# Optimization experiments

Hardware: AMD Instinct MI355X
Metric: run time of the kernel (lower is better)

Reference implementation:

```python
import jax, jax.numpy as jnp
import numpy as np

FRAME_LEN = 512
FRAME_HOP = 256
EPSILON = float(np.finfo(np.float32).eps)


def _dft_kernels(frame_len=FRAME_LEN):
    # Matches torch: K = view_as_real(fft.rfft(eye(N), dim=1))[:frame_len], windowed by hann.
    # rfft of delta at t gives exp(-2pi i f t / N): real = cos, imag = -sin.
    N = frame_len  # already a power of two
    n = jnp.arange(frame_len, dtype=jnp.float32)
    window = 0.5 * (1.0 - jnp.cos(2.0 * jnp.pi * n / frame_len))  # periodic hann
    f = jnp.arange(N // 2 + 1, dtype=jnp.float32)  # 257 bins
    ang = 2.0 * jnp.pi * f[:, None] * n[None, :] / N  # [F, L]
    Kr = jnp.cos(ang) * window
    Ki = -jnp.sin(ang) * window  # torch rfft imaginary part
    return Kr, Ki


def _frame(x, frame_len=FRAME_LEN, hop=FRAME_HOP):
    B, Ns = x.shape
    T = (Ns - frame_len) // hop + 1
    idx = jnp.arange(T)[:, None] * hop + jnp.arange(frame_len)[None, :]  # [T, L]
    return x[:, idx]  # [B, T, L]


def reference(x):
    Kr, Ki = _dft_kernels()
    xf = _frame(x)  # [B, T, L]
    r = jnp.einsum('btl,fl->bft', xf, Kr)       # real part of conv1d output
    i = -jnp.einsum('btl,fl->bft', xf, Ki)      # i = -imag (as in torch code)
    mag = jnp.sqrt(r * r + i * i)               # B x F x T
    f = jnp.clip(mag, EPSILON, None)
    mean = jnp.mean(f, axis=-1, keepdims=True)
    std = jnp.std(f, axis=-1, keepdims=True, ddof=1)  # torch std is unbiased
    feat = (f - mean) / (std + EPSILON)
    return mag, feat


def setup_inputs() -> dict:
    key = jax.random.key(0)
    x = jax.random.normal(key, (64, 160000), dtype=jnp.float32)
    return {"x": x}
```

## Files before the change

kernel.cpp:

```cpp
#include <hip/hip_runtime.h>
#include <math.h>

#define FRAME_LEN 512
#define HOP       256
#define NFREQ     257
#define NBATCH    64
#define NSAMP     160000
#define NSAMPH    80000
#define TFRAMES   624
#define EPS       1.1920928955078125e-07f

#define MT 128
#define FT 32
#define BK 64
#define KH 256
#define XBLKS 5000

#define ASZ (MT * BK)
#define BSZ (2 * FT * BK)

typedef __attribute__((ext_vector_type(8))) short short8;
typedef __attribute__((ext_vector_type(4))) float f32x4;

static __device__ __forceinline__ unsigned int f2bf(float f) {
    unsigned int u = __float_as_uint(f);
    return (u + 0x7fffu + ((u >> 16) & 1u)) >> 16;
}
static __device__ __forceinline__ void gload_lds16(const void* g, void* l) {
    __builtin_amdgcn_global_load_lds(
        (const __attribute__((address_space(1))) void*)g,
        (__attribute__((address_space(3))) void*)l, 16, 0, 0);
}

__global__ __launch_bounds__(256) void prep(const float* __restrict__ x,
                                            unsigned short* __restrict__ xe,
                                            unsigned short* __restrict__ xo,
                                            unsigned short* __restrict__ Wec,
                                            unsigned short* __restrict__ Wes,
                                            unsigned short* __restrict__ Woc,
                                            unsigned short* __restrict__ Wos) {
    if (blockIdx.x < XBLKS) {
        int i = blockIdx.x * 256 + threadIdx.x;
        const float4* src = (const float4*)x + (size_t)i * 2;
        float4 a = src[0], b = src[1];
        uint2 e, o;
        e.x = f2bf(a.x) | (f2bf(a.z) << 16);
        e.y = f2bf(b.x) | (f2bf(b.z) << 16);
        o.x = f2bf(a.y) | (f2bf(a.w) << 16);
        o.y = f2bf(b.y) | (f2bf(b.w) << 16);
        *(uint2*)(xe + (size_t)i * 4) = e;
        *(uint2*)(xo + (size_t)i * 4) = o;
    } else {
        int f = blockIdx.x - XBLKS;
        int n2 = threadIdx.x;
        unsigned short ec = 0, es = 0, oc = 0, os = 0;
        if (f <= 128) {
            int ne = 2 * n2, no = 2 * n2 + 1;
            float we = 0.5f * (1.0f - cosf(2.0f * (float)M_PI * (float)ne / (float)FRAME_LEN));
            float wo = 0.5f * (1.0f - cosf(2.0f * (float)M_PI * (float)no / (float)FRAME_LEN));
            float ange = (float)((f * ne) & (FRAME_LEN - 1)) * (2.0f * (float)M_PI / (float)FRAME_LEN);
            float ango = (float)((f * no) & (FRAME_LEN - 1)) * (2.0f * (float)M_PI / (float)FRAME_LEN);
            float se_, ce_, so_, co_;
            sincosf(ange, &se_, &ce_);
            sincosf(ango, &so_, &co_);
            ec = (unsigned short)f2bf(ce_ * we);
            es = (unsigned short)f2bf(se_ * we);
            oc = (unsigned short)f2bf(co_ * wo);
            os = (unsigned short)f2bf(so_ * wo);
        }
        Wec[f * KH + n2] = ec; Wes[f * KH + n2] = es;
        Woc[f * KH + n2] = oc; Wos[f * KH + n2] = os;
    }
}

__global__ __launch_bounds__(256) void stft_mfma(
    const unsigned short* __restrict__ xe, const unsigned short* __restrict__ xo,
    const unsigned short* __restrict__ Wec, const unsigned short* __restrict__ Wes,
    const unsigned short* __restrict__ Woc, const unsigned short* __restrict__ Wos,
    float* __restrict__ mag)
{
    __shared__ unsigned short As[2][MT][BK];
    __shared__ unsigned short Bs[2][2][FT][BK];

    const int tid = threadIdx.x;
    const int logical = ((int)blockIdx.x & 7) * 195 + ((int)blockIdx.x >> 3);
    const int tileM = logical / 5;
    const int tileF = logical % 5;
    const int wid = tid >> 6;
    const int lane = tid & 63;
    const int lrow = lane & 15;
    const int lhi = lane >> 4;

    unsigned short* AsB = &As[0][0][0];
    unsigned short* BsB = &Bs[0][0][0][0];

    const unsigned short* pA[2][4];
    #pragma unroll
    for (int j = 0; j < 4; j++) {
        int idx = wid * 4 + j;
        int row = idx * 8 + (lane >> 3);
        int m = tileM * MT + row;
        int b = m / TFRAMES;
        int t = m - b * TFRAMES;
        int chunk = (lane & 7) ^ (row & 7);
        size_t off = (size_t)b * NSAMPH + t * (HOP / 2) + chunk * 8;
        pA[0][j] = xe + off;
        pA[1][j] = xo + off;
    }
    const unsigned short* pB[2][2];
    #pragma unroll
    for (int j = 0; j < 2; j++) {
        int i = wid * 2 + j;
        int row = (i & 3) * 8 + (lane >> 3);
        int fg = tileF * FT + row;
        int chunk = (lane & 7) ^ (row & 7);
        size_t off = (size_t)fg * KH + chunk * 8;
        pB[0][j] = ((i & 4) ? Wes : Wec) + off;
        pB[1][j] = ((i & 4) ? Wos : Woc) + off;
    }

    f32x4 aC[2][2][2] = {};
    f32x4 aS[2][2][2] = {};

    #pragma unroll
    for (int j = 0; j < 4; j++)
        gload_lds16(pA[0][j], AsB + (wid * 4 + j) * 512);
    #pragma unroll
    for (int j = 0; j < 2; j++)
        gload_lds16(pB[0][j], BsB + (wid * 2 + j) * 512);
    __syncthreads();

    int buf = 0;
    #pragma unroll
    for (int it = 0; it < 8; it++) {
        const int p = it >> 2;
        if (it < 7) {
            const int pn = (it + 1) >> 2;
            const int k0 = ((it + 1) & 3) * BK;
            #pragma unroll
            for (int j = 0; j < 4; j++)
                gload_lds16(pA[pn][j] + k0, AsB + (buf ^ 1) * ASZ + (wid * 4 + j) * 512);
            #pragma unroll
            for (int j = 0; j < 2; j++)
                gload_lds16(pB[pn][j] + k0, BsB + (buf ^ 1) * BSZ + (wid * 2 + j) * 512);
        }
        #pragma unroll
        for (int ks = 0; ks < 2; ks++) {
            short8 a[2], bc[2], bsn[2];
            const int c = (ks * 4 + lhi) ^ (lrow & 7);
            #pragma unroll
            for (int mf = 0; mf < 2; mf++)
                a[mf] = *(const short8*)(AsB + buf * ASZ +
                    (wid * 32 + mf * 16 + lrow) * BK + c * 8);
            #pragma unroll
            for (int nf = 0; nf < 2; nf++) {
                bc[nf]  = *(const short8*)(BsB + buf * BSZ +
                    (nf * 16 + lrow) * BK + c * 8);
                bsn[nf] = *(const short8*)(BsB + buf * BSZ + FT * BK +
                    (nf * 16 + lrow) * BK + c * 8);
            }
            #pragma unroll
            for (int mf = 0; mf < 2; mf++) {
                #pragma unroll
                for (int nf = 0; nf < 2; nf++) {
                    aC[p][mf][nf] = __builtin_amdgcn_mfma_f32_16x16x32_bf16(
                        a[mf], bc[nf], aC[p][mf][nf], 0, 0, 0);
                    aS[p][mf][nf] = __builtin_amdgcn_mfma_f32_16x16x32_bf16(
                        a[mf], bsn[nf], aS[p][mf][nf], 0, 0, 0);
                }
            }
        }
        __syncthreads();
        buf ^= 1;
    }

    #pragma unroll
    for (int mf = 0; mf < 2; mf++) {
        int m0 = tileM * MT + wid * 32 + mf * 16 + lhi * 4;
        int b = m0 / TFRAMES;
        int t = m0 - b * TFRAMES;
        #pragma unroll
        for (int nf = 0; nf < 2; nf++) {
            int f = tileF * FT + nf * 16 + lrow;
            float4 od, om;
            #pragma unroll
            for (int q = 0; q < 4; q++) {
                const float Ce = aC[0][mf][nf][q], Co = aC[1][mf][nf][q];
                const float Se = aS[0][mf][nf][q], So = aS[1][mf][nf][q];
                const float rd = Ce + Co, id = Se + So;
                const float rm = Ce - Co, im = So - Se;
                (&od.x)[q] = sqrtf(rd * rd + id * id);
                (&om.x)[q] = sqrtf(rm * rm + im * im);
            }
            if (f <= 128)
                *(float4*)(mag + ((size_t)b * NFREQ + f) * TFRAMES + t) = od;
            if (f <= 127)
                *(float4*)(mag + ((size_t)b * NFREQ + (256 - f)) * TFRAMES + t) = om;
        }
    }
}

__global__ __launch_bounds__(256) void normalize(const float* __restrict__ mag,
                                                 float* __restrict__ feat)
{
    const int row = blockIdx.x * 4 + (threadIdx.x >> 6);
    const int lane = threadIdx.x & 63;
    const float* mp = mag + (size_t)row * TFRAMES;

    float4 v[3];
    float sum = 0.f;
    #pragma unroll
    for (int i = 0; i < 3; i++) {
        int c4 = lane + i * 64;
        if (c4 < TFRAMES / 4) {
            float4 t = *(const float4*)(mp + c4 * 4);
            t.x = fmaxf(t.x, EPS); t.y = fmaxf(t.y, EPS);
            t.z = fmaxf(t.z, EPS); t.w = fmaxf(t.w, EPS);
            v[i] = t;
            sum += (t.x + t.y) + (t.z + t.w);
        } else {
            v[i] = make_float4(0.f, 0.f, 0.f, 0.f);
        }
    }
    #pragma unroll
    for (int off = 1; off < 64; off <<= 1) sum += __shfl_xor(sum, off, 64);
    const float mean = sum * (1.0f / (float)TFRAMES);

    float ssd = 0.f;
    #pragma unroll
    for (int i = 0; i < 3; i++) {
        int c4 = lane + i * 64;
        if (c4 < TFRAMES / 4) {
            float dx = v[i].x - mean, dy = v[i].y - mean;
            float dz = v[i].z - mean, dw = v[i].w - mean;
            ssd += (dx * dx + dy * dy) + (dz * dz + dw * dw);
        }
    }
    #pragma unroll
    for (int off = 1; off < 64; off <<= 1) ssd += __shfl_xor(ssd, off, 64);
    const float stdv = sqrtf(ssd * (1.0f / (float)(TFRAMES - 1)));
    const float inv = 1.0f / (stdv + EPS);

    float* fp = feat + (size_t)row * TFRAMES;
    #pragma unroll
    for (int i = 0; i < 3; i++) {
        int c4 = lane + i * 64;
        if (c4 < TFRAMES / 4) {
            float4 o;
            o.x = (v[i].x - mean) * inv; o.y = (v[i].y - mean) * inv;
            o.z = (v[i].z - mean) * inv; o.w = (v[i].w - mean) * inv;
            *(float4*)(fp + c4 * 4) = o;
        }
    }
}

extern "C" void kernel_launch(void* const* d_in, const int* in_sizes, int n_in,
                              void* d_out, int out_size, void* d_ws, size_t ws_size,
                              hipStream_t stream) {
    const float* x = (const float*)d_in[0];
    unsigned short* Wec = (unsigned short*)d_ws;
    unsigned short* Wes = Wec + 160 * KH;
    unsigned short* Woc = Wes + 160 * KH;
    unsigned short* Wos = Woc + 160 * KH;
    unsigned short* xe  = Wos + 160 * KH;
    unsigned short* xo  = xe + (size_t)NBATCH * NSAMPH;
    float* mag  = (float*)d_out;
    float* feat = mag + (size_t)NBATCH * NFREQ * TFRAMES;

    prep<<<XBLKS + 160, 256, 0, stream>>>(x, xe, xo, Wec, Wes, Woc, Wos);

    stft_mfma<<<312 * 5, 256, 0, stream>>>(xe, xo, Wec, Wes, Woc, Wos, mag);

    normalize<<<NBATCH * NFREQ / 4, 256, 0, stream>>>(mag, feat);
}
```

Before: 54.40 us.

## Stage A tiles through registers with two-deep prefetch and widen prep conversion

The STFT GEMM kernel stops using direct global-to-LDS loads for the signal tile. It now loads the A tile into registers two iterations ahead, writes it into swizzled LDS after compute, and uses manual waitcnt and barriers so the loads overlap the MFMA work. The B tile still uses direct LDS loads, one stage ahead. The kernel also gains an occupancy hint (launch_bounds 256,3), and the bf16 prep kernel now handles 16 floats per thread with half as many blocks. This adds register pressure and relies on hand-written vmcnt counting that must match the load order exactly.

```diff
diff --git a/kernel.cpp b/kernel.cpp
--- a/kernel.cpp
+++ b/kernel.cpp
@@ -14,7 +14,7 @@
 #define FT 32
 #define BK 64
 #define KH 256
-#define XBLKS 5000
+#define XBLKS 2500
 
 #define ASZ (MT * BK)
 #define BSZ (2 * FT * BK)
@@ -41,15 +41,19 @@
                                             unsigned short* __restrict__ Wos) {
     if (blockIdx.x < XBLKS) {
         int i = blockIdx.x * 256 + threadIdx.x;
-        const float4* src = (const float4*)x + (size_t)i * 2;
-        float4 a = src[0], b = src[1];
-        uint2 e, o;
-        e.x = f2bf(a.x) | (f2bf(a.z) << 16);
-        e.y = f2bf(b.x) | (f2bf(b.z) << 16);
-        o.x = f2bf(a.y) | (f2bf(a.w) << 16);
-        o.y = f2bf(b.y) | (f2bf(b.w) << 16);
-        *(uint2*)(xe + (size_t)i * 4) = e;
-        *(uint2*)(xo + (size_t)i * 4) = o;
+        const float4* src = (const float4*)x + (size_t)i * 4;
+        float4 v0 = src[0], v1 = src[1], v2 = src[2], v3 = src[3];
+        uint4 e, o;
+        e.x = f2bf(v0.x) | (f2bf(v0.z) << 16);
+        e.y = f2bf(v1.x) | (f2bf(v1.z) << 16);
+        e.z = f2bf(v2.x) | (f2bf(v2.z) << 16);
+        e.w = f2bf(v3.x) | (f2bf(v3.z) << 16);
+        o.x = f2bf(v0.y) | (f2bf(v0.w) << 16);
+        o.y = f2bf(v1.y) | (f2bf(v1.w) << 16);
+        o.z = f2bf(v2.y) | (f2bf(v2.w) << 16);
+        o.w = f2bf(v3.y) | (f2bf(v3.w) << 16);
+        *(uint4*)(xe + (size_t)i * 8) = e;
+        *(uint4*)(xo + (size_t)i * 8) = o;
     } else {
         int f = blockIdx.x - XBLKS;
         int n2 = threadIdx.x;
@@ -73,7 +77,7 @@
     }
 }
 
-__global__ __launch_bounds__(256) void stft_mfma(
+__global__ __launch_bounds__(256, 3) void stft_mfma(
     const unsigned short* __restrict__ xe, const unsigned short* __restrict__ xo,
     const unsigned short* __restrict__ Wec, const unsigned short* __restrict__ Wes,
     const unsigned short* __restrict__ Woc, const unsigned short* __restrict__ Wos,
@@ -95,17 +99,17 @@
     unsigned short* BsB = &Bs[0][0][0][0];
 
     const unsigned short* pA[2][4];
+    int wAo[4];
     #pragma unroll
     for (int j = 0; j < 4; j++) {
-        int idx = wid * 4 + j;
-        int row = idx * 8 + (lane >> 3);
-        int m = tileM * MT + row;
+        int r = (wid * 4 + j) * 8 + (lane >> 3);
+        int m = tileM * MT + r;
         int b = m / TFRAMES;
         int t = m - b * TFRAMES;
-        int chunk = (lane & 7) ^ (row & 7);
-        size_t off = (size_t)b * NSAMPH + t * (HOP / 2) + chunk * 8;
+        size_t off = (size_t)b * NSAMPH + t * (HOP / 2) + (lane & 7) * 8;
         pA[0][j] = xe + off;
         pA[1][j] = xo + off;
+        wAo[j] = r * (BK * 2) + ((((lane & 7) ^ (r & 7))) << 4);
     }
     const unsigned short* pB[2][2];
     #pragma unroll
@@ -121,57 +125,88 @@
 
     f32x4 aC[2][2][2] = {};
     f32x4 aS[2][2][2] = {};
-
+    uint4 R0[4], R1[4];
+
+    #pragma unroll
+    for (int j = 0; j < 4; j++) R0[j] = *(const uint4*)(pA[0][j]);
+    __builtin_amdgcn_sched_barrier(0);
+    #pragma unroll
+    for (int j = 0; j < 2; j++) gload_lds16(pB[0][j], BsB + (wid * 2 + j) * 512);
+    __builtin_amdgcn_sched_barrier(0);
+    #pragma unroll
+    for (int j = 0; j < 4; j++) R1[j] = *(const uint4*)(pA[0][j] + BK);
     #pragma unroll
     for (int j = 0; j < 4; j++)
-        gload_lds16(pA[0][j], AsB + (wid * 4 + j) * 512);
-    #pragma unroll
-    for (int j = 0; j < 2; j++)
-        gload_lds16(pB[0][j], BsB + (wid * 2 + j) * 512);
-    __syncthreads();
-
-    int buf = 0;
-    #pragma unroll
-    for (int it = 0; it < 8; it++) {
-        const int p = it >> 2;
-        if (it < 7) {
-            const int pn = (it + 1) >> 2;
-            const int k0 = ((it + 1) & 3) * BK;
-            #pragma unroll
-            for (int j = 0; j < 4; j++)
-                gload_lds16(pA[pn][j] + k0, AsB + (buf ^ 1) * ASZ + (wid * 4 + j) * 512);
+        *(uint4*)((char*)AsB + wAo[j]) = R0[j];
+    asm volatile("s_waitcnt vmcnt(4) lgkmcnt(0)" ::: "memory");
+    __builtin_amdgcn_s_barrier();
+    __builtin_amdgcn_sched_barrier(0);
+
+    #pragma unroll
+    for (int c = 0; c < 8; c++) {
+        if (c + 1 < 8) {
+            const int pn = (c + 1) >> 2, kn = ((c + 1) & 3) * BK;
             #pragma unroll
             for (int j = 0; j < 2; j++)
-                gload_lds16(pB[pn][j] + k0, BsB + (buf ^ 1) * BSZ + (wid * 2 + j) * 512);
-        }
-        #pragma unroll
-        for (int ks = 0; ks < 2; ks++) {
-            short8 a[2], bc[2], bsn[2];
-            const int c = (ks * 4 + lhi) ^ (lrow & 7);
+                gload_lds16(pB[pn][j] + kn,
+                            BsB + ((c + 1) & 1) * BSZ + (wid * 2 + j) * 512);
+        }
+        __builtin_amdgcn_sched_barrier(0);
+        if (c + 2 < 8) {
+            const int p2 = (c + 2) >> 2, k2 = ((c + 2) & 3) * BK;
+            if ((c & 1) == 0) {
+                #pragma unroll
+                for (int j = 0; j < 4; j++) R0[j] = *(const uint4*)(pA[p2][j] + k2);
+            } else {
+                #pragma unroll
+                for (int j = 0; j < 4; j++) R1[j] = *(const uint4*)(pA[p2][j] + k2);
+            }
+        }
+        {
+            const int p = c >> 2, bo = c & 1;
             #pragma unroll
-            for (int mf = 0; mf < 2; mf++)
-                a[mf] = *(const short8*)(AsB + buf * ASZ +
-                    (wid * 32 + mf * 16 + lrow) * BK + c * 8);
-            #pragma unroll
-            for (int nf = 0; nf < 2; nf++) {
-                bc[nf]  = *(const short8*)(BsB + buf * BSZ +
-                    (nf * 16 + lrow) * BK + c * 8);
-                bsn[nf] = *(const short8*)(BsB + buf * BSZ + FT * BK +
-                    (nf * 16 + lrow) * BK + c * 8);
-            }
-            #pragma unroll
-            for (int mf = 0; mf < 2; mf++) {
+            for (int ks = 0; ks < 2; ks++) {
+                short8 a[2], bc[2], bsn[2];
+                const int ci = (ks * 4 + lhi) ^ (lrow & 7);
+                #pragma unroll
+                for (int mf = 0; mf < 2; mf++)
+                    a[mf] = *(const short8*)(AsB + bo * ASZ +
+                        (wid * 32 + mf * 16 + lrow) * BK + ci * 8);
                 #pragma unroll
                 for (int nf = 0; nf < 2; nf++) {
-                    aC[p][mf][nf] = __builtin_amdgcn_mfma_f32_16x16x32_bf16(
-                        a[mf], bc[nf], aC[p][mf][nf], 0, 0, 0);
-                    aS[p][mf][nf] = __builtin_amdgcn_mfma_f32_16x16x32_bf16(
-                        a[mf], bsn[nf], aS[p][mf][nf], 0, 0, 0);
+                    bc[nf]  = *(const short8*)(BsB + bo * BSZ +
+                        (nf * 16 + lrow) * BK + ci * 8);
+                    bsn[nf] = *(const short8*)(BsB + bo * BSZ + FT * BK +
+                        (nf * 16 + lrow) * BK + ci * 8);
+                }
+                #pragma unroll
+                for (int mf = 0; mf < 2; mf++) {
+                    #pragma unroll
+                    for (int nf = 0; nf < 2; nf++) {
+                        aC[p][mf][nf] = __builtin_amdgcn_mfma_f32_16x16x32_bf16(
+                            a[mf], bc[nf], aC[p][mf][nf], 0, 0, 0);
+                        aS[p][mf][nf] = __builtin_amdgcn_mfma_f32_16x16x32_bf16(
+                            a[mf], bsn[nf], aS[p][mf][nf], 0, 0, 0);
+                    }
                 }
             }
         }
-        __syncthreads();
-        buf ^= 1;
+        if (c < 7) {
+            const int wb = (c + 1) & 1;
+            if ((c & 1) == 0) {
+                #pragma unroll
+                for (int j = 0; j < 4; j++)
+                    *(uint4*)((char*)AsB + wb * (ASZ * 2) + wAo[j]) = R1[j];
+            } else {
+                #pragma unroll
+                for (int j = 0; j < 4; j++)
+                    *(uint4*)((char*)AsB + wb * (ASZ * 2) + wAo[j]) = R0[j];
+            }
+            if (c < 6) asm volatile("s_waitcnt vmcnt(4) lgkmcnt(0)" ::: "memory");
+            else       asm volatile("s_waitcnt vmcnt(0) lgkmcnt(0)" ::: "memory");
+            __builtin_amdgcn_s_barrier();
+            __builtin_amdgcn_sched_barrier(0);
+        }
     }
 
     #pragma unroll
```

New measurement: 56.76 us. +4.3%, slower.

## Drop LDS staging in STFT MFMA kernel, load fragments directly from global

Applied to the files above, without the earlier changes.

The GEMM kernel no longer double-buffers A and B tiles through shared memory with async global-to-LDS loads and barriers. Each lane instead reads its bf16 MFMA fragments straight from global memory and relies on L1/L2 for reuse across waves. This removes LDS traffic and __syncthreads, but it gives up explicit data sharing and latency hiding, and it issues redundant global reads. The prep kernel also now converts 16 floats per thread with 128-bit stores, and the window-table blocks come first.

```diff
diff --git a/kernel.cpp b/kernel.cpp
--- a/kernel.cpp
+++ b/kernel.cpp
@@ -12,12 +12,9 @@
 
 #define MT 128
 #define FT 32
-#define BK 64
 #define KH 256
-#define XBLKS 5000
-
-#define ASZ (MT * BK)
-#define BSZ (2 * FT * BK)
+#define TBLKS 160
+#define XBLKS 2500
 
 typedef __attribute__((ext_vector_type(8))) short short8;
 typedef __attribute__((ext_vector_type(4))) float f32x4;
@@ -25,11 +22,6 @@
 static __device__ __forceinline__ unsigned int f2bf(float f) {
     unsigned int u = __float_as_uint(f);
     return (u + 0x7fffu + ((u >> 16) & 1u)) >> 16;
-}
-static __device__ __forceinline__ void gload_lds16(const void* g, void* l) {
-    __builtin_amdgcn_global_load_lds(
-        (const __attribute__((address_space(1))) void*)g,
-        (__attribute__((address_space(3))) void*)l, 16, 0, 0);
 }
 
 __global__ __launch_bounds__(256) void prep(const float* __restrict__ x,
@@ -39,19 +31,8 @@
                                             unsigned short* __restrict__ Wes,
                                             unsigned short* __restrict__ Woc,
                                             unsigned short* __restrict__ Wos) {
-    if (blockIdx.x < XBLKS) {
-        int i = blockIdx.x * 256 + threadIdx.x;
-        const float4* src = (const float4*)x + (size_t)i * 2;
-        float4 a = src[0], b = src[1];
-        uint2 e, o;
-        e.x = f2bf(a.x) | (f2bf(a.z) << 16);
-        e.y = f2bf(b.x) | (f2bf(b.z) << 16);
-        o.x = f2bf(a.y) | (f2bf(a.w) << 16);
-        o.y = f2bf(b.y) | (f2bf(b.w) << 16);
-        *(uint2*)(xe + (size_t)i * 4) = e;
-        *(uint2*)(xo + (size_t)i * 4) = o;
-    } else {
-        int f = blockIdx.x - XBLKS;
+    if (blockIdx.x < TBLKS) {
+        int f = blockIdx.x;
         int n2 = threadIdx.x;
         unsigned short ec = 0, es = 0, oc = 0, os = 0;
         if (f <= 128) {
@@ -70,6 +51,21 @@
         }
         Wec[f * KH + n2] = ec; Wes[f * KH + n2] = es;
         Woc[f * KH + n2] = oc; Wos[f * KH + n2] = os;
+    } else {
+        int i = (blockIdx.x - TBLKS) * 256 + threadIdx.x;
+        const float4* src = (const float4*)x + (size_t)i * 4;
+        float4 v0 = src[0], v1 = src[1], v2 = src[2], v3 = src[3];
+        uint4 e, o;
+        e.x = f2bf(v0.x) | (f2bf(v0.z) << 16);
+        e.y = f2bf(v1.x) | (f2bf(v1.z) << 16);
+        e.z = f2bf(v2.x) | (f2bf(v2.z) << 16);
+        e.w = f2bf(v3.x) | (f2bf(v3.z) << 16);
+        o.x = f2bf(v0.y) | (f2bf(v0.w) << 16);
+        o.y = f2bf(v1.y) | (f2bf(v1.w) << 16);
+        o.z = f2bf(v2.y) | (f2bf(v2.w) << 16);
+        o.w = f2bf(v3.y) | (f2bf(v3.w) << 16);
+        *(uint4*)(xe + (size_t)i * 8) = e;
+        *(uint4*)(xo + (size_t)i * 8) = o;
     }
 }
 
@@ -79,9 +75,6 @@
     const unsigned short* __restrict__ Woc, const unsigned short* __restrict__ Wos,
     float* __restrict__ mag)
 {
-    __shared__ unsigned short As[2][MT][BK];
-    __shared__ unsigned short Bs[2][2][FT][BK];
-
     const int tid = threadIdx.x;
     const int logical = ((int)blockIdx.x & 7) * 195 + ((int)blockIdx.x >> 3);
     const int tileM = logical / 5;
@@ -91,73 +84,44 @@
     const int lrow = lane & 15;
     const int lhi = lane >> 4;
 
-    unsigned short* AsB = &As[0][0][0];
-    unsigned short* BsB = &Bs[0][0][0][0];
-
-    const unsigned short* pA[2][4];
-    #pragma unroll
-    for (int j = 0; j < 4; j++) {
-        int idx = wid * 4 + j;
-        int row = idx * 8 + (lane >> 3);
-        int m = tileM * MT + row;
+    const unsigned short* rowA[2][2];
+    #pragma unroll
+    for (int mf = 0; mf < 2; mf++) {
+        int r = wid * 32 + mf * 16 + lrow;
+        int m = tileM * MT + r;
         int b = m / TFRAMES;
         int t = m - b * TFRAMES;
-        int chunk = (lane & 7) ^ (row & 7);
-        size_t off = (size_t)b * NSAMPH + t * (HOP / 2) + chunk * 8;
-        pA[0][j] = xe + off;
-        pA[1][j] = xo + off;
-    }
-    const unsigned short* pB[2][2];
-    #pragma unroll
-    for (int j = 0; j < 2; j++) {
-        int i = wid * 2 + j;
-        int row = (i & 3) * 8 + (lane >> 3);
-        int fg = tileF * FT + row;
-        int chunk = (lane & 7) ^ (row & 7);
-        size_t off = (size_t)fg * KH + chunk * 8;
-        pB[0][j] = ((i & 4) ? Wes : Wec) + off;
-        pB[1][j] = ((i & 4) ? Wos : Woc) + off;
+        size_t off = (size_t)b * NSAMPH + t * (HOP / 2) + lhi * 8;
+        rowA[0][mf] = xe + off;
+        rowA[1][mf] = xo + off;
+    }
+    const unsigned short* rowB[2][2][2];
+    #pragma unroll
+    for (int nf = 0; nf < 2; nf++) {
+        int fg = tileF * FT + nf * 16 + lrow;
+        size_t off = (size_t)fg * KH + lhi * 8;
+        rowB[0][0][nf] = Wec + off; rowB[0][1][nf] = Wes + off;
+        rowB[1][0][nf] = Woc + off; rowB[1][1][nf] = Wos + off;
     }
 
     f32x4 aC[2][2][2] = {};
     f32x4 aS[2][2][2] = {};
 
     #pragma unroll
-    for (int j = 0; j < 4; j++)
-        gload_lds16(pA[0][j], AsB + (wid * 4 + j) * 512);
-    #pragma unroll
-    for (int j = 0; j < 2; j++)
-        gload_lds16(pB[0][j], BsB + (wid * 2 + j) * 512);
-    __syncthreads();
-
-    int buf = 0;
-    #pragma unroll
-    for (int it = 0; it < 8; it++) {
-        const int p = it >> 2;
-        if (it < 7) {
-            const int pn = (it + 1) >> 2;
-            const int k0 = ((it + 1) & 3) * BK;
-            #pragma unroll
-            for (int j = 0; j < 4; j++)
-                gload_lds16(pA[pn][j] + k0, AsB + (buf ^ 1) * ASZ + (wid * 4 + j) * 512);
-            #pragma unroll
-            for (int j = 0; j < 2; j++)
-                gload_lds16(pB[pn][j] + k0, BsB + (buf ^ 1) * BSZ + (wid * 2 + j) * 512);
-        }
+    for (int c = 0; c < 8; c++) {
+        const int p = c >> 2;
+        const int k0 = (c & 3) * 64;
         #pragma unroll
         for (int ks = 0; ks < 2; ks++) {
-            short8 a[2], bc[2], bsn[2];
-            const int c = (ks * 4 + lhi) ^ (lrow & 7);
+            const int kk = k0 + ks * 32;
+            short8 a[2], bc[2], bs[2];
             #pragma unroll
             for (int mf = 0; mf < 2; mf++)
-                a[mf] = *(const short8*)(AsB + buf * ASZ +
-                    (wid * 32 + mf * 16 + lrow) * BK + c * 8);
+                a[mf] = *(const short8*)(rowA[p][mf] + kk);
             #pragma unroll
             for (int nf = 0; nf < 2; nf++) {
-                bc[nf]  = *(const short8*)(BsB + buf * BSZ +
-                    (nf * 16 + lrow) * BK + c * 8);
-                bsn[nf] = *(const short8*)(BsB + buf * BSZ + FT * BK +
-                    (nf * 16 + lrow) * BK + c * 8);
+                bc[nf] = *(const short8*)(rowB[p][0][nf] + kk);
+                bs[nf] = *(const short8*)(rowB[p][1][nf] + kk);
             }
             #pragma unroll
             for (int mf = 0; mf < 2; mf++) {
@@ -166,12 +130,10 @@
                     aC[p][mf][nf] = __builtin_amdgcn_mfma_f32_16x16x32_bf16(
                         a[mf], bc[nf], aC[p][mf][nf], 0, 0, 0);
                     aS[p][mf][nf] = __builtin_amdgcn_mfma_f32_16x16x32_bf16(
-                        a[mf], bsn[nf], aS[p][mf][nf], 0, 0, 0);
+                        a[mf], bs[nf], aS[p][mf][nf], 0, 0, 0);
                 }
             }
         }
-        __syncthreads();
-        buf ^= 1;
     }
 
     #pragma unroll
@@ -267,7 +229,7 @@
     float* mag  = (float*)d_out;
     float* feat = mag + (size_t)NBATCH * NFREQ * TFRAMES;
 
-    prep<<<XBLKS + 160, 256, 0, stream>>>(x, xe, xo, Wec, Wes, Woc, Wos);
+    prep<<<TBLKS + XBLKS, 256, 0, stream>>>(x, xe, xo, Wec, Wes, Woc, Wos);
 
     stft_mfma<<<312 * 5, 256, 0, stream>>>(xe, xo, Wec, Wes, Woc, Wos, mag);
 
```

New measurement: 107.3 us. +97.2%, slower.

## Remap prep and normalize block indices for XCD-local batch ownership

Applied to the files above, without the earlier changes.

The prep kernel now has each thread convert 16 samples with wider stores, and maps blocks so that each XCD (block index mod 8) converts a contiguous set of 8 batches. The normalize kernel similarly remaps blocks so each XCD processes a contiguous range of rows. The intent is to improve L2 locality between producer and consumer kernels on MI355X's per-XCD caches and to reduce per-thread overhead. The risk is that the assumed block-to-XCD round-robin mapping does not hold, and that the gemm kernel's XCD mapping does not match.

```diff
diff --git a/kernel.cpp b/kernel.cpp
--- a/kernel.cpp
+++ b/kernel.cpp
@@ -14,7 +14,7 @@
 #define FT 32
 #define BK 64
 #define KH 256
-#define XBLKS 5000
+#define XBLKS 2560
 
 #define ASZ (MT * BK)
 #define BSZ (2 * FT * BK)
@@ -40,16 +40,27 @@
                                             unsigned short* __restrict__ Woc,
                                             unsigned short* __restrict__ Wos) {
     if (blockIdx.x < XBLKS) {
-        int i = blockIdx.x * 256 + threadIdx.x;
-        const float4* src = (const float4*)x + (size_t)i * 2;
-        float4 a = src[0], b = src[1];
-        uint2 e, o;
-        e.x = f2bf(a.x) | (f2bf(a.z) << 16);
-        e.y = f2bf(b.x) | (f2bf(b.z) << 16);
-        o.x = f2bf(a.y) | (f2bf(a.w) << 16);
-        o.y = f2bf(b.y) | (f2bf(b.w) << 16);
-        *(uint2*)(xe + (size_t)i * 4) = e;
-        *(uint2*)(xo + (size_t)i * 4) = o;
+        const int xcd = blockIdx.x & 7;
+        const int slot = blockIdx.x >> 3;
+        const int b = xcd * 8 + slot / 40;
+        const int within = slot % 40;
+        const int s0 = within * 4096 + threadIdx.x * 16;
+        if (s0 + 16 <= NSAMP) {
+            const float4* src = (const float4*)(x + (size_t)b * NSAMP + s0);
+            float4 v0 = src[0], v1 = src[1], v2 = src[2], v3 = src[3];
+            uint4 e, o;
+            e.x = f2bf(v0.x) | (f2bf(v0.z) << 16);
+            e.y = f2bf(v1.x) | (f2bf(v1.z) << 16);
+            e.z = f2bf(v2.x) | (f2bf(v2.z) << 16);
+            e.w = f2bf(v3.x) | (f2bf(v3.z) << 16);
+            o.x = f2bf(v0.y) | (f2bf(v0.w) << 16);
+            o.y = f2bf(v1.y) | (f2bf(v1.w) << 16);
+            o.z = f2bf(v2.y) | (f2bf(v2.w) << 16);
+            o.w = f2bf(v3.y) | (f2bf(v3.w) << 16);
+            size_t off = (size_t)b * NSAMPH + s0 / 2;
+            *(uint4*)(xe + off) = e;
+            *(uint4*)(xo + off) = o;
+        }
     } else {
         int f = blockIdx.x - XBLKS;
         int n2 = threadIdx.x;
@@ -203,7 +214,8 @@
 __global__ __launch_bounds__(256) void normalize(const float* __restrict__ mag,
                                                  float* __restrict__ feat)
 {
-    const int row = blockIdx.x * 4 + (threadIdx.x >> 6);
+    const int row4 = ((int)blockIdx.x & 7) * 514 + ((int)blockIdx.x >> 3);
+    const int row = row4 * 4 + (threadIdx.x >> 6);
     const int lane = threadIdx.x & 63;
     const float* mp = mag + (size_t)row * TFRAMES;
 
```

Measured after the change: 54.47 us. No clear change (+0.1%).
